# Kernel tuning notes

Measured on AMD Instinct MI355X. Metric: run time of the kernel, lower is better.

## Reference

```python
import jax, jax.numpy as jnp
import numpy as np

B, S, DIM = 2, 2048, 2048
N_HEADS, N_KV_HEADS = 16, 4
HEAD_DIM = DIM // N_HEADS  # 128
N_REP = N_HEADS // N_KV_HEADS  # 4


def setup_inputs() -> dict:
    key = jax.random.key(0)
    ks = jax.random.split(key, 7)
    x = jax.random.normal(ks[0], (B, S, DIM), dtype=jnp.float32)
    cos = jax.random.uniform(ks[1], (S, HEAD_DIM // 2), dtype=jnp.float32)
    sin = jax.random.uniform(ks[2], (S, HEAD_DIM // 2), dtype=jnp.float32)
    sc = 1.0 / np.sqrt(DIM)
    wq = jax.random.normal(ks[3], (DIM, N_HEADS * HEAD_DIM), dtype=jnp.float32) * sc
    wk = jax.random.normal(ks[4], (DIM, N_KV_HEADS * HEAD_DIM), dtype=jnp.float32) * sc
    wv = jax.random.normal(ks[5], (DIM, N_KV_HEADS * HEAD_DIM), dtype=jnp.float32) * sc
    wo = jax.random.normal(ks[6], (N_HEADS * HEAD_DIM, DIM), dtype=jnp.float32) * sc
    return {"x": x, "cos": cos, "sin": sin, "wq": wq, "wk": wk, "wv": wv, "wo": wo}


def _rope(t, cos, sin):
    # t: [B, S, H, hd]; cos/sin: [S, hd/2] -> broadcast as [1, S, 1, hd/2]
    tr, ti = t[..., ::2], t[..., 1::2]
    c = cos[None, :, None, :]
    s = sin[None, :, None, :]
    out_r = tr * c - ti * s
    out_i = tr * s + ti * c
    # interleave back: stack on new last axis then flatten
    return jnp.stack([out_r, out_i], axis=-1).reshape(t.shape)


def reference(x, cos, sin, wq, wk, wv, wo):
    bsz, seqlen, _ = x.shape
    xq = (x @ wq).reshape(bsz, seqlen, N_HEADS, HEAD_DIM)
    xk = (x @ wk).reshape(bsz, seqlen, N_KV_HEADS, HEAD_DIM)
    xv = (x @ wv).reshape(bsz, seqlen, N_KV_HEADS, HEAD_DIM)
    xq = _rope(xq, cos, sin)
    xk = _rope(xk, cos, sin)
    # GQA: repeat kv heads -> [B, S, H, hd]
    xk = jnp.repeat(xk, N_REP, axis=2)
    xv = jnp.repeat(xv, N_REP, axis=2)
    scale = 1.0 / jnp.sqrt(jnp.asarray(HEAD_DIM, dtype=x.dtype))
    scores = jnp.einsum("bqhd,bkhd->bhqk", xq, xk) * scale
    causal = jnp.tril(jnp.ones((seqlen, seqlen), dtype=bool))
    scores = jnp.where(causal[None, None, :, :], scores, jnp.asarray(-jnp.inf, dtype=scores.dtype))
    attn = jax.nn.softmax(scores, axis=-1)
    out = jnp.einsum("bhqk,bkhd->bqhd", attn, xv)
    out = out.reshape(bsz, seqlen, N_HEADS * HEAD_DIM)
    return out @ wo
```

## Files before the change

kernel.cpp:

```cpp
#include <hip/hip_runtime.h>
#include <stdint.h>

#define SEQ 2048

typedef uint16_t u16;
typedef uint32_t u32;
typedef __attribute__((ext_vector_type(4))) float f32x4;
typedef __attribute__((ext_vector_type(8))) __bf16 bf16x8;
typedef __attribute__((ext_vector_type(4))) __bf16 bf16x4;

__device__ __forceinline__ u16 f2bf(float f) {
    u32 u = __float_as_uint(f);
    u += 0x7FFFu + ((u >> 16) & 1u);
    return (u16)(u >> 16);
}
__device__ __forceinline__ float bf2f(u16 h) {
    return __uint_as_float(((u32)h) << 16);
}
__device__ __forceinline__ void async16(const void* g, void* l) {
    auto gp = (__attribute__((address_space(1))) void*)const_cast<void*>(g);
    auto lp = (__attribute__((address_space(3))) void*)l;
    __builtin_amdgcn_global_load_lds(gp, lp, 16, 0, 0);
}

__global__ __launch_bounds__(256) void convert_bf16(const float* __restrict__ src,
                                                    u16* __restrict__ dst) {
    int i = blockIdx.x * 256 + threadIdx.x;
    float4 v = ((const float4*)src)[i];
    u32 lo = (u32)f2bf(v.x) | ((u32)f2bf(v.y) << 16);
    u32 hi = (u32)f2bf(v.z) | ((u32)f2bf(v.w) << 16);
    ((uint2*)dst)[i] = make_uint2(lo, hi);
}

__global__ __launch_bounds__(256) void tconv(const float* __restrict__ src,
                                             u16* __restrict__ dst, int N, int K) {
    __shared__ float tile[64][65];
    const int n0 = blockIdx.x * 64, k0 = blockIdx.y * 64;
    const int tid = threadIdx.x;
#pragma unroll
    for (int p = 0; p < 4; p++) {
        int r = p * 16 + (tid >> 4);
        int c = (tid & 15) * 4;
        float4 v = *(const float4*)&src[(size_t)(k0 + r) * N + n0 + c];
        tile[r][c] = v.x; tile[r][c+1] = v.y; tile[r][c+2] = v.z; tile[r][c+3] = v.w;
    }
    __syncthreads();
#pragma unroll
    for (int p = 0; p < 4; p++) {
        int n = p * 16 + (tid >> 4);
        int kq = (tid & 15) * 4;
        u32 lo = (u32)f2bf(tile[kq+0][n]) | ((u32)f2bf(tile[kq+1][n]) << 16);
        u32 hi = (u32)f2bf(tile[kq+2][n]) | ((u32)f2bf(tile[kq+3][n]) << 16);
        *(uint2*)&dst[(size_t)(n0 + n) * K + k0 + kq] = make_uint2(lo, hi);
    }
}

template <int BN, bool F32OUT>
__global__ __launch_bounds__(512, 2) void gemm256(const u16* __restrict__ A,
                                                  const u16* __restrict__ Bt,
                                                  void* __restrict__ Cv,
                                                  int N, int K, int nbx) {
    constexpr int NF = BN / 64;
    constexpr int SLOT = 8192 + BN * 32;
    __shared__ u16 lds[4 * SLOT];

    const int nwg = gridDim.x;
    const int q = nwg >> 3, r = nwg & 7;
    const int xcd = blockIdx.x & 7, lid = blockIdx.x >> 3;
    const int wg = (xcd < r ? xcd * (q + 1) : r * (q + 1) + (xcd - r) * q) + lid;
    const int by = wg / nbx, bx = wg - by * nbx;
    const int m0 = by * 256, n0 = bx * BN;

    const int tid = threadIdx.x;
    const int w = tid >> 6, l = tid & 63;
    const int lr = l & 15, quad = l >> 4;
    const int wm = (w >> 2) * 128;
    const int wn = (w & 3) * (BN / 4);
    const int cs = (quad ^ (lr & 3)) * 8;

    const int rA = w * 32 + (l >> 2);
    const int gA = ((l & 3) ^ (rA & 3)) * 8;
    const u16* aS = A + (size_t)(m0 + rA) * K + gA;
    u16* ldA = lds + (w * 128 + l) * 8;

    const u16* bS;
    u16* ldB;
    if constexpr (BN == 256) {
        bS = Bt + (size_t)(n0 + rA) * K + gA;
        ldB = lds + 8192 + (w * 128 + l) * 8;
    } else {
        const int rB = w * 16 + (l >> 2);
        const int gB = ((l & 3) ^ (rB & 3)) * 8;
        bS = Bt + (size_t)(n0 + rB) * K + gB;
        ldB = lds + 8192 + tid * 8;
    }

    f32x4 acc[8][NF] = {};
    const int nK = K >> 5;

    auto stageA = [&](int kt) {
        u16* d = ldA + (kt & 3) * SLOT;
        const u16* s = aS + (size_t)kt * 32;
        async16(s, d);
        async16(s + (size_t)16 * K, d + 512);
    };
    auto stageB = [&](int kt) {
        u16* d = ldB + (kt & 3) * SLOT;
        const u16* s = bS + (size_t)kt * 32;
        async16(s, d);
        if constexpr (BN == 256) async16(s + (size_t)16 * K, d + 512);
    };

    stageA(0); stageB(0); stageA(1); stageB(1); stageA(2); stageB(2);
    if constexpr (BN == 256)
        asm volatile("s_waitcnt vmcnt(8)" ::: "memory");
    else
        asm volatile("s_waitcnt vmcnt(6)" ::: "memory");
    __builtin_amdgcn_s_barrier();

    for (int kt = 0; kt < nK; ++kt) {
        const u16* As = lds + (kt & 3) * SLOT;
        const u16* Bs = As + 8192;
        const bool pre = (kt + 3 < nK);
        if constexpr (BN == 256) {
            bf16x8 af[4], bfr[4];
#pragma unroll
            for (int i = 0; i < 4; i++)
                af[i] = *(const bf16x8*)&As[(wm + i * 16 + lr) * 32 + cs];
#pragma unroll
            for (int i = 0; i < 4; i++)
                bfr[i] = *(const bf16x8*)&Bs[(wn + i * 16 + lr) * 32 + cs];
            if (pre) stageA(kt + 3);
            __builtin_amdgcn_s_barrier();
            asm volatile("s_waitcnt lgkmcnt(0)" ::: "memory");
            __builtin_amdgcn_s_setprio(1);
#pragma unroll
            for (int mf = 0; mf < 4; mf++)
#pragma unroll
                for (int nf = 0; nf < 4; nf++)
                    acc[mf][nf] = __builtin_amdgcn_mfma_f32_16x16x32_bf16(af[mf], bfr[nf], acc[mf][nf], 0, 0, 0);
            __builtin_amdgcn_s_setprio(0);
            __builtin_amdgcn_s_barrier();
#pragma unroll
            for (int i = 0; i < 4; i++)
                af[i] = *(const bf16x8*)&As[(wm + 64 + i * 16 + lr) * 32 + cs];
            if (pre) stageB(kt + 3);
            __builtin_amdgcn_s_barrier();
            asm volatile("s_waitcnt lgkmcnt(0)" ::: "memory");
            __builtin_amdgcn_s_setprio(1);
#pragma unroll
            for (int mf = 0; mf < 4; mf++)
#pragma unroll
                for (int nf = 0; nf < 4; nf++)
                    acc[4 + mf][nf] = __builtin_amdgcn_mfma_f32_16x16x32_bf16(af[mf], bfr[nf], acc[4 + mf][nf], 0, 0, 0);
            __builtin_amdgcn_s_setprio(0);
            if (kt < nK - 3)       asm volatile("s_waitcnt vmcnt(8)" ::: "memory");
            else if (kt == nK - 3) asm volatile("s_waitcnt vmcnt(4)" ::: "memory");
            else if (kt == nK - 2) asm volatile("s_waitcnt vmcnt(0)" ::: "memory");
            if (kt < nK - 1) __builtin_amdgcn_s_barrier();
        } else {
            bf16x8 af[8], bfr[2];
#pragma unroll
            for (int i = 0; i < 8; i++)
                af[i] = *(const bf16x8*)&As[(wm + i * 16 + lr) * 32 + cs];
#pragma unroll
            for (int i = 0; i < 2; i++)
                bfr[i] = *(const bf16x8*)&Bs[(wn + i * 16 + lr) * 32 + cs];
            if (pre) { stageA(kt + 3); stageB(kt + 3); }
            __builtin_amdgcn_s_barrier();
            asm volatile("s_waitcnt lgkmcnt(0)" ::: "memory");
            __builtin_amdgcn_s_setprio(1);
#pragma unroll
            for (int mf = 0; mf < 8; mf++)
#pragma unroll
                for (int nf = 0; nf < 2; nf++)
                    acc[mf][nf] = __builtin_amdgcn_mfma_f32_16x16x32_bf16(af[mf], bfr[nf], acc[mf][nf], 0, 0, 0);
            __builtin_amdgcn_s_setprio(0);
            if (kt < nK - 3)       asm volatile("s_waitcnt vmcnt(6)" ::: "memory");
            else if (kt == nK - 3) asm volatile("s_waitcnt vmcnt(3)" ::: "memory");
            else if (kt == nK - 2) asm volatile("s_waitcnt vmcnt(0)" ::: "memory");
            if (kt < nK - 1) __builtin_amdgcn_s_barrier();
        }
    }

#pragma unroll
    for (int mf = 0; mf < 8; mf++) {
#pragma unroll
        for (int nf = 0; nf < NF; nf++) {
#pragma unroll
            for (int rr = 0; rr < 4; rr++) {
                size_t row = (size_t)(m0 + wm + mf * 16 + quad * 4 + rr);
                size_t col = (size_t)(n0 + wn + nf * 16 + lr);
                if (F32OUT)
                    ((float*)Cv)[row * (size_t)N + col] = acc[mf][nf][rr];
                else
                    ((u16*)Cv)[row * (size_t)N + col] = f2bf(acc[mf][nf][rr]);
            }
        }
    }
}

__global__ __launch_bounds__(256) void rope_k(u16* __restrict__ qkv,
                                              const float* __restrict__ cosp,
                                              const float* __restrict__ sinp) {
    const int t = blockIdx.x;
    const int spos = t & (SEQ - 1);
    const int tid = threadIdx.x;
    u16* row = qkv + (size_t)t * 3072;
    const int col = 2048 + 2 * tid;
    const int ci = tid & 63;
    u32 v = *(u32*)(row + col);
    float tr = bf2f((u16)(v & 0xFFFFu));
    float ti = bf2f((u16)(v >> 16));
    float cs = cosp[spos * 64 + ci];
    float sn = sinp[spos * 64 + ci];
    float orr = tr * cs - ti * sn;
    float oi  = tr * sn + ti * cs;
    *(u32*)(row + col) = (u32)f2bf(orr) | ((u32)f2bf(oi) << 16);
}

__global__ __launch_bounds__(256) void transpose_v(const u16* __restrict__ qkv,
                                                   u16* __restrict__ vt) {
    __shared__ u16 tile[64][65];
    const int bid = blockIdx.x;
    const int dt = bid & 1;
    const int st = (bid >> 1) & 31;
    const int kh = (bid >> 6) & 3;
    const int b  = bid >> 8;
    const int tid = threadIdx.x;
#pragma unroll
    for (int pp = 0; pp < 2; pp++) {
        int r  = pp * 32 + (tid >> 3);
        int c8 = (tid & 7) * 8;
        const u16* src = qkv + (size_t)(b * SEQ + st * 64 + r) * 3072 + 2560 + kh * 128 + dt * 64 + c8;
        uint4 v = *(const uint4*)src;
        tile[r][c8+0] = (u16)(v.x & 0xFFFF); tile[r][c8+1] = (u16)(v.x >> 16);
        tile[r][c8+2] = (u16)(v.y & 0xFFFF); tile[r][c8+3] = (u16)(v.y >> 16);
        tile[r][c8+4] = (u16)(v.z & 0xFFFF); tile[r][c8+5] = (u16)(v.z >> 16);
        tile[r][c8+6] = (u16)(v.w & 0xFFFF); tile[r][c8+7] = (u16)(v.w >> 16);
    }
    __syncthreads();
#pragma unroll
    for (int pp = 0; pp < 2; pp++) {
        int dr = pp * 32 + (tid >> 3);
        int s8 = (tid & 7) * 8;
        uint4 o;
        o.x = (u32)tile[s8+0][dr] | ((u32)tile[s8+1][dr] << 16);
        o.y = (u32)tile[s8+2][dr] | ((u32)tile[s8+3][dr] << 16);
        o.z = (u32)tile[s8+4][dr] | ((u32)tile[s8+5][dr] << 16);
        o.w = (u32)tile[s8+6][dr] | ((u32)tile[s8+7][dr] << 16);
        u16* dst = vt + ((size_t)((b * 4 + kh) * 128 + dt * 64 + dr)) * SEQ + st * 64 + s8;
        *(uint4*)dst = o;
    }
}

__global__ __launch_bounds__(512, 2) void flash_attn(const u16* __restrict__ qkv,
                                                     const u16* __restrict__ vt,
                                                     const float* __restrict__ cosp,
                                                     const float* __restrict__ sinp,
                                                     u16* __restrict__ ob) {
    __shared__ u16 sh[49152];
    const int bidx = blockIdx.x;
    const int a  = bidx & 7;
    const int bh = bidx >> 3;
    const int b = bh >> 4, h = bh & 15, kh = h >> 2;
    const int tid = threadIdx.x;
    const int w = tid >> 6, lane = tid & 63;
    const int grp = w >> 2, wl = w & 3;
    const int lr = lane & 15, quad = lane >> 4;
    const float qscale = 0.088388347762f * 1.4426950408889634f;

    u16* lKg = sh + grp * 16384;
    u16* lVg = lKg + 8192;
    u16* lPw = sh + 32768 + w * 2048;

    const int tidg = tid & 255;
    const int krow = tidg >> 4;
    const int kchunk = (tidg & 15) ^ krow;
    const int vrow = tidg >> 3;
    const int vchunk = (tidg & 7) ^ (vrow & 7);
    const u16* kRow = qkv + (size_t)b * SEQ * 3072 + 2048 + kh * 128
                    + (size_t)krow * 3072 + kchunk * 8;
    const u16* vRow = vt + (size_t)(b * 4 + kh) * 128 * SEQ
                    + (size_t)vrow * SEQ + vchunk * 8;
    u16* lKd = lKg + tidg * 8;
    u16* lVd = lVg + tidg * 8;

    float* mO = (float*)sh;
    float* mM = (float*)(sh + 32768);

    for (int p = 0; p < 2; p++) {
        const int qt = p ? (7 - a) : (8 + a);
        const int niters = p ? (8 - a) : (9 + a);
        const int kt0 = grp * niters;

        bf16x8 qf[2][4];
#pragma unroll
        for (int qi = 0; qi < 2; qi++) {
            const int token = qt * 128 + wl * 32 + qi * 16 + lr;
            const u16* qb = qkv + (size_t)(b * SEQ + token) * 3072 + h * 128;
#pragma unroll
            for (int kk = 0; kk < 4; kk++) {
                uint4 raw = *(const uint4*)(qb + kk * 32 + quad * 8);
                u32 rw[4] = {raw.x, raw.y, raw.z, raw.w};
                union { u16 us[8]; bf16x8 v; } fr;
#pragma unroll
                for (int pp = 0; pp < 4; pp++) {
                    int ci = kk * 16 + quad * 4 + pp;
                    float cv = cosp[token * 64 + ci];
                    float sv = sinp[token * 64 + ci];
                    float tr = bf2f((u16)(rw[pp] & 0xFFFFu));
                    float ti = bf2f((u16)(rw[pp] >> 16));
                    fr.us[2 * pp]     = f2bf((tr * cv - ti * sv) * qscale);
                    fr.us[2 * pp + 1] = f2bf((tr * sv + ti * cv) * qscale);
                }
                qf[qi][kk] = fr.v;
            }
        }

        f32x4 o[2][8] = {};
        float m_st[2] = {-1e30f, -1e30f};
        float l_st[2] = {0.f, 0.f};
        const int qg = qt * 128 + wl * 32 + lr;

        for (int t = 0; t < niters; t++) {
            const int kt = kt0 + t;
#pragma unroll
            for (int i = 0; i < 4; i++)
                async16(kRow + (size_t)(kt * 64 + i * 16) * 3072, lKd + i * 2048);
#pragma unroll
            for (int i = 0; i < 4; i++)
                async16(vRow + (size_t)(i * 32) * SEQ + kt * 64, lVd + i * 2048);
            asm volatile("s_waitcnt vmcnt(0)" ::: "memory");
            asm volatile("s_barrier" ::: "memory");

            f32x4 sc[2][4] = {};
#pragma unroll
            for (int nf = 0; nf < 4; nf++) {
#pragma unroll
                for (int kk = 0; kk < 4; kk++) {
                    bf16x8 ak = *(const bf16x8*)&lKg[(nf * 16 + lr) * 128 + (((kk * 4 + quad) ^ lr) * 8)];
                    sc[0][nf] = __builtin_amdgcn_mfma_f32_16x16x32_bf16(ak, qf[0][kk], sc[0][nf], 0, 0, 0);
                    sc[1][nf] = __builtin_amdgcn_mfma_f32_16x16x32_bf16(ak, qf[1][kk], sc[1][nf], 0, 0, 0);
                }
            }

            const int kb = kt * 64 + quad * 4;
            const int kmax = kt * 64 + 63;
#pragma unroll
            for (int qi = 0; qi < 2; qi++) {
                float ps[4][4];
                float tmax = -1e30f;
                const int qrow_g = qg + qi * 16;
                if (kmax > qt * 128 + wl * 32 + qi * 16) {
#pragma unroll
                    for (int nf = 0; nf < 4; nf++)
#pragma unroll
                        for (int r = 0; r < 4; r++) {
                            float v = sc[qi][nf][r];
                            if ((kb + nf * 16 + r) > qrow_g) v = -1e30f;
                            ps[nf][r] = v;
                            tmax = fmaxf(tmax, v);
                        }
                } else {
#pragma unroll
                    for (int nf = 0; nf < 4; nf++)
#pragma unroll
                        for (int r = 0; r < 4; r++) {
                            float v = sc[qi][nf][r];
                            ps[nf][r] = v;
                            tmax = fmaxf(tmax, v);
                        }
                }
                tmax = fmaxf(tmax, __shfl_xor(tmax, 16));
                tmax = fmaxf(tmax, __shfl_xor(tmax, 32));
                const float mprev = m_st[qi];
                if (!__all(tmax - mprev <= 8.0f)) {
                    float mnew = fmaxf(mprev, tmax);
                    float alpha = exp2f(mprev - mnew);
                    l_st[qi] *= alpha;
                    m_st[qi] = mnew;
#pragma unroll
                    for (int r = 0; r < 4; r++) {
                        float ar = __shfl(alpha, quad * 4 + r, 16);
#pragma unroll
                        for (int nd = 0; nd < 8; nd++) o[qi][nd][r] *= ar;
                    }
                }
                const float mcur = m_st[qi];
                float rsum = 0.f;
#pragma unroll
                for (int nf = 0; nf < 4; nf++)
#pragma unroll
                    for (int r = 0; r < 4; r++) {
                        float e = exp2f(ps[nf][r] - mcur);
                        ps[nf][r] = e;
                        rsum += e;
                    }
                rsum += __shfl_xor(rsum, 16);
                rsum += __shfl_xor(rsum, 32);
                l_st[qi] += rsum;
                const int qrow = qi * 16 + lr;
#pragma unroll
                for (int nf = 0; nf < 4; nf++) {
                    u32 lo = (u32)f2bf(ps[nf][0]) | ((u32)f2bf(ps[nf][1]) << 16);
                    u32 hi = (u32)f2bf(ps[nf][2]) | ((u32)f2bf(ps[nf][3]) << 16);
                    int c = (nf * 4 + quad) ^ lr;
                    *(uint2*)&lPw[qrow * 64 + c * 4] = make_uint2(lo, hi);
                }
            }

#pragma unroll
            for (int kf = 0; kf < 2; kf++) {
                bf16x8 pa[2];
#pragma unroll
                for (int qi = 0; qi < 2; qi++) {
                    int c0 = (kf * 8 + quad * 2) ^ lr;
                    int c1 = (kf * 8 + quad * 2 + 1) ^ lr;
                    bf16x4 p0 = *(const bf16x4*)&lPw[(qi * 16 + lr) * 64 + c0 * 4];
                    bf16x4 p1 = *(const bf16x4*)&lPw[(qi * 16 + lr) * 64 + c1 * 4];
                    pa[qi] = __builtin_shufflevector(p0, p1, 0, 1, 2, 3, 4, 5, 6, 7);
                }
#pragma unroll
                for (int nd = 0; nd < 8; nd++) {
                    bf16x8 vb = *(const bf16x8*)&lVg[(nd * 16 + lr) * 64 + (((kf * 4 + quad) ^ (lr & 7)) * 8)];
                    o[0][nd] = __builtin_amdgcn_mfma_f32_16x16x32_bf16(pa[0], vb, o[0][nd], 0, 0, 0);
                    o[1][nd] = __builtin_amdgcn_mfma_f32_16x16x32_bf16(pa[1], vb, o[1][nd], 0, 0, 0);
                }
            }

            asm volatile("s_barrier" ::: "memory");
        }

        __syncthreads();
        if (grp == 1) {
#pragma unroll
            for (int qi = 0; qi < 2; qi++) {
#pragma unroll
                for (int r = 0; r < 4; r++) {
                    int row = wl * 32 + qi * 16 + quad * 4 + r;
#pragma unroll
                    for (int nd = 0; nd < 8; nd++)
                        mO[row * 128 + nd * 16 + lr] = o[qi][nd][r];
                }
                if (quad == 0) {
                    int rowl = wl * 32 + qi * 16 + lr;
                    mM[rowl * 2]     = m_st[qi];
                    mM[rowl * 2 + 1] = l_st[qi];
                }
            }
        }
        __syncthreads();
        if (grp == 0) {
#pragma unroll
            for (int qi = 0; qi < 2; qi++) {
                int rowl = wl * 32 + qi * 16 + lr;
                float m1 = mM[rowl * 2], l1 = mM[rowl * 2 + 1];
                float M  = fmaxf(m_st[qi], m1);
                float a0 = exp2f(m_st[qi] - M);
                float a1 = exp2f(m1 - M);
                float li = 1.0f / (l_st[qi] * a0 + l1 * a1);
                u16* obase = ob + (size_t)(b * SEQ + qt * 128 + wl * 32 + qi * 16) * 2048 + h * 128;
#pragma unroll
                for (int r = 0; r < 4; r++) {
                    float a0b = __shfl(a0, quad * 4 + r, 16);
                    float a1b = __shfl(a1, quad * 4 + r, 16);
                    float lib = __shfl(li, quad * 4 + r, 16);
                    int row = wl * 32 + qi * 16 + quad * 4 + r;
#pragma unroll
                    for (int nd = 0; nd < 8; nd++) {
                        float val = (o[qi][nd][r] * a0b + mO[row * 128 + nd * 16 + lr] * a1b) * lib;
                        obase[(quad * 4 + r) * 2048 + nd * 16 + lr] = f2bf(val);
                    }
                }
            }
        }
        __syncthreads();
    }
}

extern "C" void kernel_launch(void* const* d_in, const int* in_sizes, int n_in,
                              void* d_out, int out_size, void* d_ws, size_t ws_size,
                              hipStream_t stream) {
    (void)in_sizes; (void)n_in; (void)out_size; (void)ws_size;
    const float* x    = (const float*)d_in[0];
    const float* cosp = (const float*)d_in[1];
    const float* sinp = (const float*)d_in[2];
    const float* wq   = (const float*)d_in[3];
    const float* wk   = (const float*)d_in[4];
    const float* wv   = (const float*)d_in[5];
    const float* wo   = (const float*)d_in[6];
    float* out = (float*)d_out;

    char* ws = (char*)d_ws;
    u16* xb    = (u16*)(ws);
    u16* qkvb  = (u16*)(ws + (size_t)16 * 1024 * 1024);
    u16* wqkvT = (u16*)(ws + (size_t)40 * 1024 * 1024);
    u16* woT   = (u16*)(ws + (size_t)52 * 1024 * 1024);
    u16* vtb   = (u16*)(ws + (size_t)60 * 1024 * 1024);
    u16* ob    = xb;

    convert_bf16<<<8192, 256, 0, stream>>>(x, xb);
    tconv<<<dim3(32, 32), 256, 0, stream>>>(wq, wqkvT, 2048, 2048);
    tconv<<<dim3( 8, 32), 256, 0, stream>>>(wk, wqkvT + (size_t)2048 * 2048, 512, 2048);
    tconv<<<dim3( 8, 32), 256, 0, stream>>>(wv, wqkvT + (size_t)2560 * 2048, 512, 2048);
    tconv<<<dim3(32, 32), 256, 0, stream>>>(wo, woT, 2048, 2048);
    gemm256<256, false><<<192, 512, 0, stream>>>(xb, wqkvT, (void*)qkvb, 3072, 2048, 12);
    rope_k<<<4096, 256, 0, stream>>>(qkvb, cosp, sinp);
    transpose_v<<<512, 256, 0, stream>>>(qkvb, vtb);
    flash_attn<<<256, 512, 0, stream>>>(qkvb, vtb, cosp, sinp, ob);
    gemm256<128, true><<<256, 512, 0, stream>>>(ob, woT, (void*)out, 2048, 2048, 16);
}
```

Measured before the change: 327.8 us.

## Merge weight conversion launches, restructure GEMM warp tiling, double-buffer K in attention

The four weight transpose-convert launches become one kernel that picks its source by block index, saving launch overhead. The GEMM k-loop is unified into a single phase per iteration with square 64x64 warp tiles for the BN=128 case, removing a mid-iteration barrier pair in the BN=256 path. Flash attention now double-buffers K tiles and loads V asynchronously while QK^T and softmax run, and it raises MFMA priority. The attention block-to-head mapping also changes so that blocks sharing a KV head sit on the same XCD, for better L2 reuse. The cost is more LDS per block (64K u16) and more register pressure in the GEMM.

After: 316.4 us. 1.04x faster.

```diff
diff --git a/kernel.cpp b/kernel.cpp
--- a/kernel.cpp
+++ b/kernel.cpp
@@ -32,10 +32,19 @@
     ((uint2*)dst)[i] = make_uint2(lo, hi);
 }
 
-__global__ __launch_bounds__(256) void tconv(const float* __restrict__ src,
-                                             u16* __restrict__ dst, int N, int K) {
+__global__ __launch_bounds__(256) void tconv_all(const float* __restrict__ wq,
+                                                 const float* __restrict__ wk,
+                                                 const float* __restrict__ wv,
+                                                 const float* __restrict__ wo,
+                                                 u16* __restrict__ wqkvT,
+                                                 u16* __restrict__ woT) {
     __shared__ float tile[64][65];
-    const int n0 = blockIdx.x * 64, k0 = blockIdx.y * 64;
+    const int bx = blockIdx.x, k0 = blockIdx.y * 64;
+    const float* src; u16* dst; int N, n0;
+    if (bx < 32)      { src = wq; dst = wqkvT;                        N = 2048; n0 = bx * 64; }
+    else if (bx < 40) { src = wk; dst = wqkvT + (size_t)2048 * 2048;  N = 512;  n0 = (bx - 32) * 64; }
+    else if (bx < 48) { src = wv; dst = wqkvT + (size_t)2560 * 2048;  N = 512;  n0 = (bx - 40) * 64; }
+    else              { src = wo; dst = woT;                          N = 2048; n0 = (bx - 48) * 64; }
     const int tid = threadIdx.x;
 #pragma unroll
     for (int p = 0; p < 4; p++) {
@@ -51,7 +60,7 @@
         int kq = (tid & 15) * 4;
         u32 lo = (u32)f2bf(tile[kq+0][n]) | ((u32)f2bf(tile[kq+1][n]) << 16);
         u32 hi = (u32)f2bf(tile[kq+2][n]) | ((u32)f2bf(tile[kq+3][n]) << 16);
-        *(uint2*)&dst[(size_t)(n0 + n) * K + k0 + kq] = make_uint2(lo, hi);
+        *(uint2*)&dst[(size_t)(n0 + n) * 2048 + k0 + kq] = make_uint2(lo, hi);
     }
 }
 
@@ -60,7 +69,7 @@
                                                   const u16* __restrict__ Bt,
                                                   void* __restrict__ Cv,
                                                   int N, int K, int nbx) {
-    constexpr int NF = BN / 64;
+    constexpr int MF = (BN == 256) ? 8 : 4;
     constexpr int SLOT = 8192 + BN * 32;
     __shared__ u16 lds[4 * SLOT];
 
@@ -74,8 +83,8 @@
     const int tid = threadIdx.x;
     const int w = tid >> 6, l = tid & 63;
     const int lr = l & 15, quad = l >> 4;
-    const int wm = (w >> 2) * 128;
-    const int wn = (w & 3) * (BN / 4);
+    const int wm = (BN == 256) ? (w >> 2) * 128 : (w >> 1) * 64;
+    const int wn = (BN == 256) ? (w & 3) * 64  : (w & 1) * 64;
     const int cs = (quad ^ (lr & 3)) * 8;
 
     const int rA = w * 32 + (l >> 2);
@@ -95,7 +104,7 @@
         ldB = lds + 8192 + tid * 8;
     }
 
-    f32x4 acc[8][NF] = {};
+    f32x4 acc[MF][4] = {};
     const int nK = K >> 5;
 
     auto stageA = [&](int kt) {
@@ -122,71 +131,39 @@
         const u16* As = lds + (kt & 3) * SLOT;
         const u16* Bs = As + 8192;
         const bool pre = (kt + 3 < nK);
+        bf16x8 af[MF], bfr[4];
+#pragma unroll
+        for (int i = 0; i < MF; i++)
+            af[i] = *(const bf16x8*)&As[(wm + i * 16 + lr) * 32 + cs];
+#pragma unroll
+        for (int i = 0; i < 4; i++)
+            bfr[i] = *(const bf16x8*)&Bs[(wn + i * 16 + lr) * 32 + cs];
+        if (pre) { stageA(kt + 3); stageB(kt + 3); }
+        __builtin_amdgcn_s_barrier();
+        asm volatile("s_waitcnt lgkmcnt(0)" ::: "memory");
+        __builtin_amdgcn_s_setprio(1);
+#pragma unroll
+        for (int mf = 0; mf < MF; mf++)
+#pragma unroll
+            for (int nf = 0; nf < 4; nf++)
+                acc[mf][nf] = __builtin_amdgcn_mfma_f32_16x16x32_bf16(af[mf], bfr[nf], acc[mf][nf], 0, 0, 0);
+        __builtin_amdgcn_s_setprio(0);
         if constexpr (BN == 256) {
-            bf16x8 af[4], bfr[4];
-#pragma unroll
-            for (int i = 0; i < 4; i++)
-                af[i] = *(const bf16x8*)&As[(wm + i * 16 + lr) * 32 + cs];
-#pragma unroll
-            for (int i = 0; i < 4; i++)
-                bfr[i] = *(const bf16x8*)&Bs[(wn + i * 16 + lr) * 32 + cs];
-            if (pre) stageA(kt + 3);
-            __builtin_amdgcn_s_barrier();
-            asm volatile("s_waitcnt lgkmcnt(0)" ::: "memory");
-            __builtin_amdgcn_s_setprio(1);
-#pragma unroll
-            for (int mf = 0; mf < 4; mf++)
-#pragma unroll
-                for (int nf = 0; nf < 4; nf++)
-                    acc[mf][nf] = __builtin_amdgcn_mfma_f32_16x16x32_bf16(af[mf], bfr[nf], acc[mf][nf], 0, 0, 0);
-            __builtin_amdgcn_s_setprio(0);
-            __builtin_amdgcn_s_barrier();
-#pragma unroll
-            for (int i = 0; i < 4; i++)
-                af[i] = *(const bf16x8*)&As[(wm + 64 + i * 16 + lr) * 32 + cs];
-            if (pre) stageB(kt + 3);
-            __builtin_amdgcn_s_barrier();
-            asm volatile("s_waitcnt lgkmcnt(0)" ::: "memory");
-            __builtin_amdgcn_s_setprio(1);
-#pragma unroll
-            for (int mf = 0; mf < 4; mf++)
-#pragma unroll
-                for (int nf = 0; nf < 4; nf++)
-                    acc[4 + mf][nf] = __builtin_amdgcn_mfma_f32_16x16x32_bf16(af[mf], bfr[nf], acc[4 + mf][nf], 0, 0, 0);
-            __builtin_amdgcn_s_setprio(0);
             if (kt < nK - 3)       asm volatile("s_waitcnt vmcnt(8)" ::: "memory");
             else if (kt == nK - 3) asm volatile("s_waitcnt vmcnt(4)" ::: "memory");
             else if (kt == nK - 2) asm volatile("s_waitcnt vmcnt(0)" ::: "memory");
-            if (kt < nK - 1) __builtin_amdgcn_s_barrier();
         } else {
-            bf16x8 af[8], bfr[2];
-#pragma unroll
-            for (int i = 0; i < 8; i++)
-                af[i] = *(const bf16x8*)&As[(wm + i * 16 + lr) * 32 + cs];
-#pragma unroll
-            for (int i = 0; i < 2; i++)
-                bfr[i] = *(const bf16x8*)&Bs[(wn + i * 16 + lr) * 32 + cs];
-            if (pre) { stageA(kt + 3); stageB(kt + 3); }
-            __builtin_amdgcn_s_barrier();
-            asm volatile("s_waitcnt lgkmcnt(0)" ::: "memory");
-            __builtin_amdgcn_s_setprio(1);
-#pragma unroll
-            for (int mf = 0; mf < 8; mf++)
-#pragma unroll
-                for (int nf = 0; nf < 2; nf++)
-                    acc[mf][nf] = __builtin_amdgcn_mfma_f32_16x16x32_bf16(af[mf], bfr[nf], acc[mf][nf], 0, 0, 0);
-            __builtin_amdgcn_s_setprio(0);
             if (kt < nK - 3)       asm volatile("s_waitcnt vmcnt(6)" ::: "memory");
             else if (kt == nK - 3) asm volatile("s_waitcnt vmcnt(3)" ::: "memory");
             else if (kt == nK - 2) asm volatile("s_waitcnt vmcnt(0)" ::: "memory");
-            if (kt < nK - 1) __builtin_amdgcn_s_barrier();
         }
-    }
-
-#pragma unroll
-    for (int mf = 0; mf < 8; mf++) {
-#pragma unroll
-        for (int nf = 0; nf < NF; nf++) {
+        if (kt < nK - 1) __builtin_amdgcn_s_barrier();
+    }
+
+#pragma unroll
+    for (int mf = 0; mf < MF; mf++) {
+#pragma unroll
+        for (int nf = 0; nf < 4; nf++) {
 #pragma unroll
             for (int rr = 0; rr < 4; rr++) {
                 size_t row = (size_t)(m0 + wm + mf * 16 + quad * 4 + rr);
@@ -259,20 +236,22 @@
                                                      const float* __restrict__ cosp,
                                                      const float* __restrict__ sinp,
                                                      u16* __restrict__ ob) {
-    __shared__ u16 sh[49152];
+    __shared__ u16 sh[65536];
     const int bidx = blockIdx.x;
-    const int a  = bidx & 7;
-    const int bh = bidx >> 3;
-    const int b = bh >> 4, h = bh & 15, kh = h >> 2;
+    const int xcd   = bidx & 7;
+    const int inner = bidx >> 3;
+    const int b  = xcd >> 2, kh = xcd & 3;
+    const int h  = kh * 4 + (inner & 3);
+    const int a  = inner >> 2;
     const int tid = threadIdx.x;
     const int w = tid >> 6, lane = tid & 63;
     const int grp = w >> 2, wl = w & 3;
     const int lr = lane & 15, quad = lane >> 4;
     const float qscale = 0.088388347762f * 1.4426950408889634f;
 
-    u16* lKg = sh + grp * 16384;
-    u16* lVg = lKg + 8192;
-    u16* lPw = sh + 32768 + w * 2048;
+    u16* base_g = sh + grp * 24576;
+    u16* vb  = base_g + 16384;
+    u16* lPw = sh + 49152 + w * 2048;
 
     const int tidg = tid & 255;
     const int krow = tidg >> 4;
@@ -283,16 +262,29 @@
                     + (size_t)krow * 3072 + kchunk * 8;
     const u16* vRow = vt + (size_t)(b * 4 + kh) * 128 * SEQ
                     + (size_t)vrow * SEQ + vchunk * 8;
-    u16* lKd = lKg + tidg * 8;
-    u16* lVd = lVg + tidg * 8;
+
+    auto stageK = [&](int kt, int buf) {
+        u16* d = base_g + buf * 8192 + tidg * 8;
+#pragma unroll
+        for (int i = 0; i < 4; i++)
+            async16(kRow + (size_t)(kt * 64 + i * 16) * 3072, d + i * 2048);
+    };
+    auto stageV = [&](int kt) {
+        u16* d = vb + tidg * 8;
+#pragma unroll
+        for (int i = 0; i < 4; i++)
+            async16(vRow + (size_t)(i * 32) * SEQ + kt * 64, d + i * 2048);
+    };
 
     float* mO = (float*)sh;
-    float* mM = (float*)(sh + 32768);
+    float* mM = (float*)(sh + 49152);
 
     for (int p = 0; p < 2; p++) {
         const int qt = p ? (7 - a) : (8 + a);
         const int niters = p ? (8 - a) : (9 + a);
         const int kt0 = grp * niters;
+
+        stageK(kt0, 0);
 
         bf16x8 qf[2][4];
 #pragma unroll
@@ -325,25 +317,29 @@
 
         for (int t = 0; t < niters; t++) {
             const int kt = kt0 + t;
-#pragma unroll
-            for (int i = 0; i < 4; i++)
-                async16(kRow + (size_t)(kt * 64 + i * 16) * 3072, lKd + i * 2048);
-#pragma unroll
-            for (int i = 0; i < 4; i++)
-                async16(vRow + (size_t)(i * 32) * SEQ + kt * 64, lVd + i * 2048);
-            asm volatile("s_waitcnt vmcnt(0)" ::: "memory");
+            const int buf = t & 1;
+            stageV(kt);
+            if (t + 1 < niters) {
+                stageK(kt + 1, buf ^ 1);
+                asm volatile("s_waitcnt vmcnt(8)" ::: "memory");
+            } else {
+                asm volatile("s_waitcnt vmcnt(4)" ::: "memory");
+            }
             asm volatile("s_barrier" ::: "memory");
 
+            const u16* kcur = base_g + buf * 8192;
             f32x4 sc[2][4] = {};
+            __builtin_amdgcn_s_setprio(1);
 #pragma unroll
             for (int nf = 0; nf < 4; nf++) {
 #pragma unroll
                 for (int kk = 0; kk < 4; kk++) {
-                    bf16x8 ak = *(const bf16x8*)&lKg[(nf * 16 + lr) * 128 + (((kk * 4 + quad) ^ lr) * 8)];
+                    bf16x8 ak = *(const bf16x8*)&kcur[(nf * 16 + lr) * 128 + (((kk * 4 + quad) ^ lr) * 8)];
                     sc[0][nf] = __builtin_amdgcn_mfma_f32_16x16x32_bf16(ak, qf[0][kk], sc[0][nf], 0, 0, 0);
                     sc[1][nf] = __builtin_amdgcn_mfma_f32_16x16x32_bf16(ak, qf[1][kk], sc[1][nf], 0, 0, 0);
                 }
             }
+            __builtin_amdgcn_s_setprio(0);
 
             const int kb = kt * 64 + quad * 4;
             const int kmax = kt * 64 + 63;
@@ -410,6 +406,11 @@
                 }
             }
 
+            if (t + 1 < niters) asm volatile("s_waitcnt vmcnt(4)" ::: "memory");
+            else                asm volatile("s_waitcnt vmcnt(0)" ::: "memory");
+            asm volatile("s_barrier" ::: "memory");
+
+            __builtin_amdgcn_s_setprio(1);
 #pragma unroll
             for (int kf = 0; kf < 2; kf++) {
                 bf16x8 pa[2];
@@ -423,11 +424,12 @@
                 }
 #pragma unroll
                 for (int nd = 0; nd < 8; nd++) {
-                    bf16x8 vb = *(const bf16x8*)&lVg[(nd * 16 + lr) * 64 + (((kf * 4 + quad) ^ (lr & 7)) * 8)];
-                    o[0][nd] = __builtin_amdgcn_mfma_f32_16x16x32_bf16(pa[0], vb, o[0][nd], 0, 0, 0);
-                    o[1][nd] = __builtin_amdgcn_mfma_f32_16x16x32_bf16(pa[1], vb, o[1][nd], 0, 0, 0);
-                }
-            }
+                    bf16x8 vv = *(const bf16x8*)&vb[(nd * 16 + lr) * 64 + (((kf * 4 + quad) ^ (lr & 7)) * 8)];
+                    o[0][nd] = __builtin_amdgcn_mfma_f32_16x16x32_bf16(pa[0], vv, o[0][nd], 0, 0, 0);
+                    o[1][nd] = __builtin_amdgcn_mfma_f32_16x16x32_bf16(pa[1], vv, o[1][nd], 0, 0, 0);
+                }
+            }
+            __builtin_amdgcn_s_setprio(0);
 
             asm volatile("s_barrier" ::: "memory");
         }
@@ -501,10 +503,7 @@
     u16* ob    = xb;
 
     convert_bf16<<<8192, 256, 0, stream>>>(x, xb);
-    tconv<<<dim3(32, 32), 256, 0, stream>>>(wq, wqkvT, 2048, 2048);
-    tconv<<<dim3( 8, 32), 256, 0, stream>>>(wk, wqkvT + (size_t)2048 * 2048, 512, 2048);
-    tconv<<<dim3( 8, 32), 256, 0, stream>>>(wv, wqkvT + (size_t)2560 * 2048, 512, 2048);
-    tconv<<<dim3(32, 32), 256, 0, stream>>>(wo, woT, 2048, 2048);
+    tconv_all<<<dim3(80, 32), 256, 0, stream>>>(wq, wk, wv, wo, wqkvT, woT);
     gemm256<256, false><<<192, 512, 0, stream>>>(xb, wqkvT, (void*)qkvb, 3072, 2048, 12);
     rope_k<<<4096, 256, 0, stream>>>(qkvb, cosp, sinp);
     transpose_v<<<512, 256, 0, stream>>>(qkvb, vtb);
```
